# Performance work log

Hardware: AMD Instinct MI355X
Metric: run time of the kernel (lower is better)

Reference implementation:

```python
import jax, jax.numpy as jnp
import numpy as np


def _lstm(x, Wih, Whh, bih, bhh):
    # x: [T,B,E] -> outputs [T,B,H]; torch gate order i,f,g,o
    B = x.shape[1]
    H = Whh.shape[1]
    bias = bih + bhh
    def step(carry, xt):
        h, c = carry
        g = xt @ Wih.T + h @ Whh.T + bias  # [B,4H]
        i, f, gg, o = jnp.split(g, 4, axis=-1)
        c = jax.nn.sigmoid(f) * c + jax.nn.sigmoid(i) * jnp.tanh(gg)
        h = jax.nn.sigmoid(o) * jnp.tanh(c)
        return (h, c), h
    init = (jnp.zeros((B, H), x.dtype), jnp.zeros((B, H), x.dtype))
    _, hs = jax.lax.scan(step, init, x)
    return hs


def setup_inputs():
    key = jax.random.key(0)
    ks = jax.random.split(key, 16)
    B, T, V, NT, E, H = 128, 512, 50000, 24, 128, 256
    Hd = H // 2  # per-direction hidden
    s = 0.08
    x = jax.random.randint(ks[0], (B, T), 0, V)
    tags = jax.random.randint(ks[1], (B, T), 0, NT)
    lengths = jax.random.randint(ks[2], (B,), T // 2, T + 1)
    mask = jnp.arange(T)[None, :] < lengths[:, None]  # [B,T] bool, position 0 always valid
    emb = (jax.random.normal(ks[3], (V, E)) * s).at[0].set(0.0)  # padding_idx=0 row zeroed
    Wih_f = jax.random.normal(ks[4], (4 * Hd, E)) * s
    Whh_f = jax.random.normal(ks[5], (4 * Hd, Hd)) * s
    bih_f = jax.random.normal(ks[6], (4 * Hd,)) * s
    bhh_f = jax.random.normal(ks[7], (4 * Hd,)) * s
    Wih_b = jax.random.normal(ks[8], (4 * Hd, E)) * s
    Whh_b = jax.random.normal(ks[9], (4 * Hd, Hd)) * s
    bih_b = jax.random.normal(ks[10], (4 * Hd,)) * s
    bhh_b = jax.random.normal(ks[11], (4 * Hd,)) * s
    W_out = jax.random.normal(ks[12], (NT, H)) * s
    b_out = jnp.zeros((NT,))
    transitions = jax.random.normal(ks[13], (NT, NT))
    start_trans = jax.random.normal(ks[14], (NT,))
    end_trans = jax.random.normal(ks[15], (NT,))
    return {"x": x, "tags": tags, "mask": mask, "emb": emb,
            "Wih_f": Wih_f, "Whh_f": Whh_f, "bih_f": bih_f, "bhh_f": bhh_f,
            "Wih_b": Wih_b, "Whh_b": Whh_b, "bih_b": bih_b, "bhh_b": bhh_b,
            "W_out": W_out, "b_out": b_out, "transitions": transitions,
            "start_trans": start_trans, "end_trans": end_trans}


def reference(x, tags, mask, emb, Wih_f, Whh_f, bih_f, bhh_f,
              Wih_b, Whh_b, bih_b, bhh_b, W_out, b_out,
              transitions, start_trans, end_trans):
    # --- emissions (dropout is identity in eval) ---
    xe = emb[x]                       # [B,T,E]
    xt = xe.transpose(1, 0, 2)        # [T,B,E]
    hf = _lstm(xt, Wih_f, Whh_f, bih_f, bhh_f)               # [T,B,Hd]
    hb = _lstm(xt[::-1], Wih_b, Whh_b, bih_b, bhh_b)[::-1]   # [T,B,Hd]
    h = jnp.concatenate([hf, hb], axis=-1).transpose(1, 0, 2)  # [B,T,H]
    emissions = h @ W_out.T + b_out   # [B,T,NT]

    # --- CRF forward algorithm (logZ) via scan over time ---
    score0 = start_trans + emissions[:, 0]  # [B,NT]
    em_rest = emissions[:, 1:].transpose(1, 0, 2)  # [T-1,B,NT]
    m_rest = mask[:, 1:].T                        # [T-1,B]
    def fwd_step(score, inp):
        em_t, m_t = inp
        ns = jax.nn.logsumexp(score[:, :, None] + transitions[None] + em_t[:, None, :], axis=1)
        return jnp.where(m_t[:, None], ns, score), None
    score, _ = jax.lax.scan(fwd_step, score0, (em_rest, m_rest))
    logZ = jax.nn.logsumexp(score + end_trans, axis=1)  # [B]

    # --- gold path score, fully vectorized ---
    mf = mask.astype(emissions.dtype)
    emit = jnp.take_along_axis(emissions, tags[:, :, None], axis=2)[:, :, 0]  # [B,T]
    trans = transitions[tags[:, :-1], tags[:, 1:]]                            # [B,T-1]
    gold = start_trans[tags[:, 0]] + emit[:, 0] + jnp.sum((trans + emit[:, 1:]) * mf[:, 1:], axis=1)
    last_idx = mask.sum(axis=1) - 1
    last_tags = jnp.take_along_axis(tags, last_idx[:, None], axis=1)[:, 0]
    gold = gold + end_trans[last_tags]

    return jnp.mean(logZ - gold)
```

## Files before the change

### kernel.cpp

```cpp
#include <hip/hip_runtime.h>
#include <hip/hip_bf16.h>

typedef unsigned short u16;
typedef unsigned int   u32;
typedef _Float16 half2_t __attribute__((ext_vector_type(2)));
typedef short    bf16x8 __attribute__((ext_vector_type(8)));
typedef float    f32x4  __attribute__((ext_vector_type(4)));
typedef u32      u32x4v __attribute__((ext_vector_type(4)));

#define TT   512

__device__ __forceinline__ float sigf(float x)  { return 1.0f / (1.0f + __expf(-x)); }
__device__ __forceinline__ float tanhf_(float x){ return 1.0f - 2.0f / (__expf(2.0f * x) + 1.0f); }

__device__ __forceinline__ u16 f2bf(float x) {
  __hip_bfloat16 h = __float2bfloat16(x);
  return *reinterpret_cast<u16*>(&h);
}
__device__ __forceinline__ float bf2f(u16 u) { return __uint_as_float(((u32)u) << 16); }
__device__ __forceinline__ u32 pk2(float a, float b) {
  return (u32)f2bf(a) | ((u32)f2bf(b) << 16);
}
__device__ __forceinline__ u16 f2h(float x) {
  _Float16 h = (_Float16)x;
  union { _Float16 f; u16 u; } c; c.f = h; return c.u;
}
__device__ __forceinline__ half2_t u2h2(u32 v) {
  union { u32 u; half2_t h; } c; c.u = v; return c.h;
}

__global__ __launch_bounds__(256) void prep_k(
    const float* __restrict__ Wih_f, const float* __restrict__ Wih_b,
    const float* __restrict__ Whh_f, const float* __restrict__ Whh_b,
    const float* __restrict__ bih_f, const float* __restrict__ bhh_f,
    const float* __restrict__ bih_b, const float* __restrict__ bhh_b,
    const float* __restrict__ W_out,
    u16* __restrict__ Wb, u16* __restrict__ Whhb, float* __restrict__ bias,
    u32* __restrict__ Wout16)
{
  int i = blockIdx.x * 256 + threadIdx.x;
  {
    int n = i >> 7, k = i & 127;
    int d = n >> 9, rem = n & 511, uu = rem >> 2, g = rem & 3;
    const float* W = d ? Wih_b : Wih_f;
    Wb[i] = f2bf(W[(g * 128 + uu) * 128 + k]);
  }
  {
    int d = i >> 16, rem = i & 65535, n = rem >> 7, k = rem & 127;
    const float* W = d ? Whh_b : Whh_f;
    Whhb[i] = f2bf(W[n * 128 + k]);
  }
  if (i < 1024) {
    int d = i >> 9, rem = i & 511, uu = rem >> 2, g = rem & 3;
    int src = g * 128 + uu;
    bias[i] = d ? (bih_b[src] + bhh_b[src]) : (bih_f[src] + bhh_f[src]);
  }
  if (i < 3072) {
    Wout16[i] = (u32)f2h(W_out[2 * i]) | ((u32)f2h(W_out[2 * i + 1]) << 16);
  }
}

__global__ __launch_bounds__(256) void embed_k(
    const int* __restrict__ x, const float* __restrict__ emb, u16* __restrict__ xe)
{
  const int tid = threadIdx.x;
  const int r = blockIdx.x * 8 + (tid >> 5);
  const int lane = tid & 31;
  int token = x[r];
  float4 v = *(const float4*)&emb[(size_t)token * 128 + lane * 4];
  uint2 p; p.x = pk2(v.x, v.y); p.y = pk2(v.z, v.w);
  *(uint2*)&xe[(size_t)r * 128 + lane * 4] = p;
}

__global__ __launch_bounds__(256, 2) void gates_mfma_k(
    const u16* __restrict__ xe, const u16* __restrict__ Wb,
    const float* __restrict__ bias, u16* __restrict__ Gout)
{
  const int tid = threadIdx.x;
  const int wid = tid >> 6, l = tid & 63;
  const int wm = wid >> 1, wn = wid & 1;
  const int M0 = blockIdx.y * 128, N0 = blockIdx.x * 128;
  const int lr = l & 15, lk = l >> 4;

  f32x4 acc[4][4];
#pragma unroll
  for (int i = 0; i < 4; ++i)
#pragma unroll
    for (int j = 0; j < 4; ++j) acc[i][j] = (f32x4){0.f, 0.f, 0.f, 0.f};

#pragma unroll
  for (int ks = 0; ks < 4; ++ks) {
    bf16x8 a[4], b[4];
#pragma unroll
    for (int mi = 0; mi < 4; ++mi)
      a[mi] = *(const bf16x8*)&xe[(size_t)(M0 + wm * 64 + mi * 16 + lr) * 128 + ks * 32 + lk * 8];
#pragma unroll
    for (int ni = 0; ni < 4; ++ni)
      b[ni] = *(const bf16x8*)&Wb[(size_t)(N0 + wn * 64 + ni * 16 + lr) * 128 + ks * 32 + lk * 8];
#pragma unroll
    for (int mi = 0; mi < 4; ++mi)
#pragma unroll
      for (int ni = 0; ni < 4; ++ni)
        acc[mi][ni] = __builtin_amdgcn_mfma_f32_16x16x32_bf16(a[mi], b[ni], acc[mi][ni], 0, 0, 0);
  }

  float bcol[4];
#pragma unroll
  for (int ni = 0; ni < 4; ++ni) bcol[ni] = bias[N0 + wn * 64 + ni * 16 + lr];

  __shared__ u16 cs[128][136];
#pragma unroll
  for (int mi = 0; mi < 4; ++mi)
#pragma unroll
    for (int ni = 0; ni < 4; ++ni) {
      int col = wn * 64 + ni * 16 + lr;
#pragma unroll
      for (int r = 0; r < 4; ++r) {
        int row = wm * 64 + mi * 16 + lk * 4 + r;
        cs[row][col] = f2bf(acc[mi][ni][r] + bcol[ni]);
      }
    }
  __syncthreads();
  {
    int row = tid >> 1, c0 = (tid & 1) * 64;
    u16* dst = &Gout[(size_t)(M0 + row) * 1024 + N0 + c0];
#pragma unroll
    for (int q = 0; q < 8; ++q)
      *(uint4*)&dst[q * 8] = *(const uint4*)&cs[row][c0 + q * 8];
  }
}

__global__ __launch_bounds__(512, 1) void lstm_mfma_k(
    const u16* __restrict__ G, const u16* __restrict__ Whhb,
    u16* __restrict__ Hout)
{
  const int bid = blockIdx.x;
  const int dir = bid & 1;
  const int grp = bid >> 1;
  const int tid = threadIdx.x;
  const int w = tid >> 6, l = tid & 63;
  const int lr = l & 15, lk = l >> 4;
  const int u = 16 * w + lr;

  const u16* wbase = Whhb + ((size_t)dir << 16);
  bf16x8 B[4][4];
#pragma unroll
  for (int g = 0; g < 4; ++g)
#pragma unroll
    for (int ks = 0; ks < 4; ++ks)
      B[g][ks] = *(const bf16x8*)&wbase[(size_t)(g * 128 + u) * 128 + ks * 32 + lk * 8];

  __shared__ u16   hl[2][16][136];
  __shared__ float pg[4][516];

  for (int i = tid; i < 2 * 16 * 136; i += 512) ((u16*)hl)[i] = 0;

  const int cs_ = tid >> 7;
  const int cu  = tid & 127;
  float cc = 0.f;

  const int ts = dir ? -1 : 1;
  const int t0 = dir ? (TT - 1) : 0;
  const long gstride = (long)ts * 1024;
  const long hstride = (long)ts * 256;

  const u16* gptr = G + ((size_t)(grp * 4 + cs_) * 512 + t0) * 1024 + dir * 512 + cu * 4;
  u16*       hptr = Hout + ((size_t)(grp * 4 + cs_) * 512 + t0) * 256 + dir * 128 + cu;

  u16 hprev = 0;
  __syncthreads();

  for (int s = 0; s < TT; ++s) {
    const int cb = s & 1, wb = cb ^ 1;

    ushort4 q = *(const ushort4*)gptr;
    gptr += gstride;
    if (s > 0) { *hptr = hprev; hptr += hstride; }

    bf16x8 A[4];
#pragma unroll
    for (int ks = 0; ks < 4; ++ks)
      A[ks] = *(const bf16x8*)&hl[cb][lr][ks * 32 + lk * 8];
    f32x4 acc[4];
#pragma unroll
    for (int g = 0; g < 4; ++g) acc[g] = (f32x4){0.f, 0.f, 0.f, 0.f};
#pragma unroll
    for (int ks = 0; ks < 4; ++ks)
#pragma unroll
      for (int g = 0; g < 4; ++g)
        acc[g] = __builtin_amdgcn_mfma_f32_16x16x32_bf16(A[ks], B[g][ks], acc[g], 0, 0, 0);

    if (lk == 0) {
#pragma unroll
      for (int r = 0; r < 4; ++r) {
        f32x4 tv = (f32x4){acc[0][r], acc[1][r], acc[2][r], acc[3][r]};
        *(f32x4*)&pg[r][u * 4] = tv;
      }
    }
    __syncthreads();

    f32x4 a = *(const f32x4*)&pg[cs_][cu * 4];
    float gi = a.x + bf2f(q.x), gf = a.y + bf2f(q.y);
    float gg = a.z + bf2f(q.z), go = a.w + bf2f(q.w);
    float iv = sigf(gi), fv = sigf(gf), gv = tanhf_(gg), ov = sigf(go);
    cc = fv * cc + iv * gv;
    float hv = ov * tanhf_(cc);
    hl[wb][cs_][cu] = f2bf(hv);
    hprev = f2h(hv);
    __syncthreads();
  }
  *hptr = hprev;
}

__global__ __launch_bounds__(256) void emis_k(
    const u16* __restrict__ Hb, const u32* __restrict__ Wout16,
    const float* __restrict__ b_out, float* __restrict__ em)
{
  __shared__ __align__(16) u32 wl2[24 * 128];
  __shared__ float bo[24];
  const int tid = threadIdx.x;
  for (int i = tid; i < 3072; i += 256) wl2[i] = Wout16[i];
  if (tid < 24) bo[tid] = b_out[tid];
  __syncthreads();

  const int m = blockIdx.x * 256 + tid;
  float acc[24];
#pragma unroll
  for (int tg = 0; tg < 24; ++tg) acc[tg] = bo[tg];

  const u32* h2 = (const u32*)(Hb + (size_t)m * 256);
  for (int ck = 0; ck < 16; ++ck) {
    uint4 hv = *(const uint4*)(h2 + ck * 4);
#pragma unroll
    for (int tg = 0; tg < 24; ++tg) {
      u32x4v wv = *(const u32x4v*)&wl2[tg * 128 + ck * 4];
      float a = acc[tg];
      a = __builtin_amdgcn_fdot2(u2h2(hv.x), u2h2(wv.x), a, false);
      a = __builtin_amdgcn_fdot2(u2h2(hv.y), u2h2(wv.y), a, false);
      a = __builtin_amdgcn_fdot2(u2h2(hv.z), u2h2(wv.z), a, false);
      a = __builtin_amdgcn_fdot2(u2h2(hv.w), u2h2(wv.w), a, false);
      acc[tg] = a;
    }
  }
#pragma unroll
  for (int t6 = 0; t6 < 6; ++t6) {
    float4 o;
    o.x = acc[t6*4+0]; o.y = acc[t6*4+1]; o.z = acc[t6*4+2]; o.w = acc[t6*4+3];
    *(float4*)&em[(size_t)m * 24 + t6 * 4] = o;
  }
}

__device__ __forceinline__ int get_mask(const void* mp, int idx, bool byte_mode) {
  return byte_mode ? (int)((const unsigned char*)mp)[idx] : ((const int*)mp)[idx];
}

__global__ __launch_bounds__(64) void crf_k(
    const float* __restrict__ em, const int* __restrict__ tags,
    const void* __restrict__ maskp, const float* __restrict__ trans,
    const float* __restrict__ start_tr, const float* __restrict__ end_tr,
    float* __restrict__ out)
{
  const int b = blockIdx.x;
  const int tid = threadIdx.x;
  const bool byte_mode = (*(const u32*)maskp != 1u);
  const bool act = (tid < 48);
  const int j  = (tid < 24) ? tid : (act ? tid - 24 : 0);
  const int i0 = (tid < 24) ? 0 : 12;
  const int partner = (tid < 24) ? tid + 24 : tid - 24;

  int cnt = 0;
  for (int t = tid; t < TT; t += 64) cnt += get_mask(maskp, b * TT + t, byte_mode);
#pragma unroll
  for (int off = 32; off > 0; off >>= 1) cnt += __shfl_down(cnt, off);
  cnt = __shfl(cnt, 0);

  float Texp[12];
  if (act) {
#pragma unroll
    for (int k = 0; k < 12; ++k) Texp[k] = __expf(trans[(i0 + k) * 24 + j]);
  } else {
#pragma unroll
    for (int k = 0; k < 12; ++k) Texp[k] = 0.f;
  }

  float sc0 = act ? (start_tr[j] + em[(size_t)(b * TT) * 24 + j]) : -1e30f;
  float m = sc0;
#pragma unroll
  for (int off = 32; off > 0; off >>= 1) m = fmaxf(m, __shfl_xor(m, off));
  float P = act ? __expf(sc0 - m) : 0.f;
  float logC = m;

  float em_next = 0.f;
  if (act && cnt > 1) em_next = em[(size_t)(b * TT + 1) * 24 + j];

  for (int t = 1; t < cnt; ++t) {
    float em_cur = em_next;
    if (act && t + 1 < cnt) em_next = em[(size_t)(b * TT + t + 1) * 24 + j];

    float s0 = 0.f, s1 = 0.f, s2 = 0.f;
#pragma unroll
    for (int k = 0; k < 4; ++k)  s0 += __shfl(P, i0 + k)     * Texp[k];
#pragma unroll
    for (int k = 4; k < 8; ++k)  s1 += __shfl(P, i0 + k)     * Texp[k];
#pragma unroll
    for (int k = 8; k < 12; ++k) s2 += __shfl(P, i0 + k)     * Texp[k];
    float sh = (s0 + s1) + s2;
    float so = __shfl(sh, partner);
    float tot = sh + so;
    P = act ? (__expf(em_cur) * tot) : 0.f;

    if ((t & 3) == 0) {
      float mm = P;
#pragma unroll
      for (int off = 32; off > 0; off >>= 1) mm = fmaxf(mm, __shfl_xor(mm, off));
      P = P / mm;
      logC += __logf(mm);
    }
  }

  float z = (tid < 24) ? P * __expf(end_tr[tid]) : 0.f;
#pragma unroll
  for (int off = 32; off > 0; off >>= 1) z += __shfl_xor(z, off);
  float lzv = logC + __logf(z);

  float part = 0.f;
  for (int t = tid; t < TT; t += 64) {
    if (t >= 1 && t < cnt) {
      int tp = tags[b * TT + t - 1], tc = tags[b * TT + t];
      part += trans[tp * 24 + tc] + em[((size_t)(b * TT + t)) * 24 + tc];
    }
  }
#pragma unroll
  for (int off = 32; off > 0; off >>= 1) part += __shfl_down(part, off);
  if (tid == 0) {
    int t0g = tags[b * TT];
    float gold = start_tr[t0g] + em[(size_t)(b * TT) * 24 + t0g] + part;
    gold += end_tr[tags[b * TT + cnt - 1]];
    atomicAdd(out, (lzv - gold) * (1.0f / 128.0f));
  }
}

extern "C" void kernel_launch(void* const* d_in, const int* in_sizes, int n_in,
                              void* d_out, int out_size, void* d_ws, size_t ws_size,
                              hipStream_t stream) {
  const int*   x     = (const int*)d_in[0];
  const int*   tags  = (const int*)d_in[1];
  const void*  mask  = d_in[2];
  const float* emb   = (const float*)d_in[3];
  const float* Wih_f = (const float*)d_in[4];
  const float* Whh_f = (const float*)d_in[5];
  const float* bih_f = (const float*)d_in[6];
  const float* bhh_f = (const float*)d_in[7];
  const float* Wih_b = (const float*)d_in[8];
  const float* Whh_b = (const float*)d_in[9];
  const float* bih_b = (const float*)d_in[10];
  const float* bhh_b = (const float*)d_in[11];
  const float* W_out = (const float*)d_in[12];
  const float* b_out = (const float*)d_in[13];
  const float* trans = (const float*)d_in[14];
  const float* st_tr = (const float*)d_in[15];
  const float* en_tr = (const float*)d_in[16];

  u16*   Gb     = (u16*)d_ws;
  u16*   Hb     = Gb + (size_t)65536 * 1024;
  float* em     = (float*)(Hb + (size_t)65536 * 256);
  float* bias   = em + (size_t)65536 * 24;
  u16*   Wb     = (u16*)(bias + 1024);
  u16*   Whhb   = Wb + 131072;
  u32*   Wout16 = (u32*)(Whhb + 131072);
  u16*   xe     = Hb;

  prep_k<<<512, 256, 0, stream>>>(Wih_f, Wih_b, Whh_f, Whh_b,
                                  bih_f, bhh_f, bih_b, bhh_b, W_out,
                                  Wb, Whhb, bias, Wout16);
  embed_k<<<8192, 256, 0, stream>>>(x, emb, xe);
  gates_mfma_k<<<dim3(8, 512), 256, 0, stream>>>(xe, Wb, bias, Gb);
  lstm_mfma_k<<<64, 512, 0, stream>>>(Gb, Whhb, Hb);
  emis_k<<<256, 256, 0, stream>>>(Hb, Wout16, b_out, em);
  (void)hipMemsetAsync(d_out, 0, sizeof(float), stream);
  crf_k<<<128, 64, 0, stream>>>(em, tags, mask, trans, st_tr, en_tr, (float*)d_out);
}
```

Measured before the change: 741.6 us.

## Run one batch row per LSTM block and fuse gate math into MFMA lanes

The recurrent LSTM kernel now launches one block per (direction, batch row), 256 blocks instead of 64 blocks that each handled four batch rows. The gate nonlinearities are computed directly in the lanes that hold MFMA results, which removes the shared-memory gate staging buffer and one barrier per step. The precomputed input-gate values for the next step are prefetched one iteration ahead. The aim is a shorter serial per-step latency and more CUs in use, at the cost of 16-row MFMAs where only one row is real, so most of the matrix work is wasted, and each weight set is loaded by four times as many blocks.

```diff
diff --git a/kernel.cpp b/kernel.cpp
--- a/kernel.cpp
+++ b/kernel.cpp
@@ -135,8 +135,8 @@
     u16* __restrict__ Hout)
 {
   const int bid = blockIdx.x;
-  const int dir = bid & 1;
-  const int grp = bid >> 1;
+  const int dir = bid >> 7;
+  const int b   = bid & 127;
   const int tid = threadIdx.x;
   const int w = tid >> 6, l = tid & 63;
   const int lr = l & 15, lk = l >> 4;
@@ -150,32 +150,30 @@
     for (int ks = 0; ks < 4; ++ks)
       B[g][ks] = *(const bf16x8*)&wbase[(size_t)(g * 128 + u) * 128 + ks * 32 + lk * 8];
 
-  __shared__ u16   hl[2][16][136];
-  __shared__ float pg[4][516];
+  __shared__ u16 hl[2][16][136];
 
   for (int i = tid; i < 2 * 16 * 136; i += 512) ((u16*)hl)[i] = 0;
 
-  const int cs_ = tid >> 7;
-  const int cu  = tid & 127;
   float cc = 0.f;
-
   const int ts = dir ? -1 : 1;
   const int t0 = dir ? (TT - 1) : 0;
   const long gstride = (long)ts * 1024;
   const long hstride = (long)ts * 256;
 
-  const u16* gptr = G + ((size_t)(grp * 4 + cs_) * 512 + t0) * 1024 + dir * 512 + cu * 4;
-  u16*       hptr = Hout + ((size_t)(grp * 4 + cs_) * 512 + t0) * 256 + dir * 128 + cu;
-
+  const u16* gptr = G + ((size_t)b * 512 + t0) * 1024 + dir * 512 + u * 4;
+  u16*       hptr = Hout + ((size_t)b * 512 + t0) * 256 + dir * 128 + u;
+
+  ushort4 qcur = *(const ushort4*)gptr;
+  gptr += gstride;
   u16 hprev = 0;
   __syncthreads();
 
   for (int s = 0; s < TT; ++s) {
     const int cb = s & 1, wb = cb ^ 1;
 
-    ushort4 q = *(const ushort4*)gptr;
-    gptr += gstride;
-    if (s > 0) { *hptr = hprev; hptr += hstride; }
+    ushort4 qnext = qcur;
+    if (s + 1 < TT) { qnext = *(const ushort4*)gptr; gptr += gstride; }
+    if (s > 0)      { *hptr = hprev; hptr += hstride; }
 
     bf16x8 A[4];
 #pragma unroll
@@ -191,25 +189,20 @@
         acc[g] = __builtin_amdgcn_mfma_f32_16x16x32_bf16(A[ks], B[g][ks], acc[g], 0, 0, 0);
 
     if (lk == 0) {
-#pragma unroll
-      for (int r = 0; r < 4; ++r) {
-        f32x4 tv = (f32x4){acc[0][r], acc[1][r], acc[2][r], acc[3][r]};
-        *(f32x4*)&pg[r][u * 4] = tv;
-      }
+      float gi = acc[0][0] + bf2f(qcur.x);
+      float gf = acc[1][0] + bf2f(qcur.y);
+      float gg = acc[2][0] + bf2f(qcur.z);
+      float go = acc[3][0] + bf2f(qcur.w);
+      float iv = sigf(gi), fv = sigf(gf), gv = tanhf_(gg), ov = sigf(go);
+      cc = fv * cc + iv * gv;
+      float hv = ov * tanhf_(cc);
+      hl[wb][0][u] = f2bf(hv);
+      hprev = f2h(hv);
     }
     __syncthreads();
-
-    f32x4 a = *(const f32x4*)&pg[cs_][cu * 4];
-    float gi = a.x + bf2f(q.x), gf = a.y + bf2f(q.y);
-    float gg = a.z + bf2f(q.z), go = a.w + bf2f(q.w);
-    float iv = sigf(gi), fv = sigf(gf), gv = tanhf_(gg), ov = sigf(go);
-    cc = fv * cc + iv * gv;
-    float hv = ov * tanhf_(cc);
-    hl[wb][cs_][cu] = f2bf(hv);
-    hprev = f2h(hv);
-    __syncthreads();
-  }
-  *hptr = hprev;
+    qcur = qnext;
+  }
+  if (lk == 0) *hptr = hprev;
 }
 
 __global__ __launch_bounds__(256) void emis_k(
@@ -375,7 +368,7 @@
                                   Wb, Whhb, bias, Wout16);
   embed_k<<<8192, 256, 0, stream>>>(x, emb, xe);
   gates_mfma_k<<<dim3(8, 512), 256, 0, stream>>>(xe, Wb, bias, Gb);
-  lstm_mfma_k<<<64, 512, 0, stream>>>(Gb, Whhb, Hb);
+  lstm_mfma_k<<<256, 512, 0, stream>>>(Gb, Whhb, Hb);
   emis_k<<<256, 256, 0, stream>>>(Hb, Wout16, b_out, em);
   (void)hipMemsetAsync(d_out, 0, sizeof(float), stream);
   crf_k<<<128, 64, 0, stream>>>(em, tags, mask, trans, st_tr, en_tr, (float*)d_out);
```

New measurement: 596.7 us. 19.5% less time.
